# Performance work log

Measured on AMD Instinct MI355X. Metric: run time of the kernel, lower is better.

Reference implementation:

```python
import jax, jax.numpy as jnp
import numpy as np

DIM = 1024
NUM_HEADS = 16
HEAD_DIM = DIM // NUM_HEADS
SCALE = HEAD_DIM ** -0.5


def setup_inputs() -> dict:
    key = jax.random.key(0)
    k1, k2, k3 = jax.random.split(key, 3)
    B, N = 2, 2048
    x = jax.random.normal(k1, (B, N, DIM), dtype=jnp.float32)
    w_qkv = jax.random.normal(k2, (3 * DIM, DIM), dtype=jnp.float32) * (DIM ** -0.5)
    w_proj = jax.random.normal(k3, (DIM, DIM), dtype=jnp.float32) * (DIM ** -0.5)
    b_proj = jnp.zeros((DIM,), dtype=jnp.float32)
    return {"x": x, "w_qkv": w_qkv, "w_proj": w_proj, "b_proj": b_proj}


def reference(x, w_qkv, w_proj, b_proj):
    B, N, C = x.shape
    # qkv projection (no bias): [B,N,3C] -> [3,B,H,N,Dh]
    qkv = jnp.einsum('bnc,dc->bnd', x, w_qkv)
    qkv = qkv.reshape(B, N, 3, NUM_HEADS, HEAD_DIM).transpose(2, 0, 3, 1, 4)
    q, k, v = qkv[0], qkv[1], qkv[2]
    # scaled dot-product attention (full score matrix, as in source)
    attn = jnp.einsum('bhnd,bhmd->bhnm', q * SCALE, k)
    attn = jax.nn.softmax(attn, axis=-1)
    out = jnp.einsum('bhnm,bhmd->bhnd', attn, v)  # [B,H,N,Dh]
    out = out.transpose(0, 2, 1, 3).reshape(B, N, C)
    return out @ w_proj.T + b_proj
```

## Files before the change

kernel.cpp:

```cpp
#include <hip/hip_runtime.h>

#define DIM   1024
#define NH    16
#define HD    64
#define BATCH 2
#define SEQ   2048
#define MTOT  4096
#define SCALE 0.125f
#define LOG2E 1.44269504088896340736f

typedef __attribute__((ext_vector_type(8))) _Float16 half8_t;
typedef __attribute__((ext_vector_type(4))) _Float16 half4_t;
typedef __attribute__((ext_vector_type(2))) __fp16 pk16x2_t;
typedef __attribute__((ext_vector_type(4))) float f32x4;

union H4 { pk16x2_t h2[2]; half4_t h4; ushort4 us; };

__device__ __forceinline__ float4 ld4(const float* p) { return *(const float4*)p; }

__device__ __forceinline__ unsigned short f2h(float f) {
    _Float16 h = (_Float16)f;
    return *(unsigned short*)&h;
}

__device__ __forceinline__ float fast_exp2(float x) {
#if __has_builtin(__builtin_amdgcn_exp2f)
    return __builtin_amdgcn_exp2f(x);
#else
    return exp2f(x);
#endif
}

__device__ __forceinline__ void gl2lds16(const void* g, void* l) {
    __builtin_amdgcn_global_load_lds(
        (const __attribute__((address_space(1))) unsigned int*)g,
        (__attribute__((address_space(3))) unsigned int*)l, 16, 0, 0);
}

__global__ __launch_bounds__(256) void cvt3(const float* __restrict__ x,
                                            const float* __restrict__ wq,
                                            const float* __restrict__ wp,
                                            unsigned short* __restrict__ xh,
                                            unsigned short* __restrict__ wqh,
                                            unsigned short* __restrict__ wph) {
    size_t i = ((size_t)blockIdx.x * 256 + threadIdx.x) * 4;
    if (i < (size_t)MTOT * DIM) {
        float4 t = ld4(x + i);
        ushort4 o = {f2h(t.x), f2h(t.y), f2h(t.z), f2h(t.w)};
        *(ushort4*)(xh + i) = o;
    }
    if (i < (size_t)3 * DIM * DIM) {
        float4 t = ld4(wq + i);
        ushort4 o = {f2h(t.x), f2h(t.y), f2h(t.z), f2h(t.w)};
        *(ushort4*)(wqh + i) = o;
    }
    if (i < (size_t)DIM * DIM) {
        float4 t = ld4(wp + i);
        ushort4 o = {f2h(t.x), f2h(t.y), f2h(t.z), f2h(t.w)};
        *(ushort4*)(wph + i) = o;
    }
}

__device__ __forceinline__ void gemm128_core(const unsigned short* __restrict__ A,
                                             const unsigned short* __restrict__ B,
                                             int m0, int n0, int K,
                                             unsigned short* As, unsigned short* Bs,
                                             f32x4 acc[4][4]) {
    const int tid  = threadIdx.x;
    const int w    = tid >> 6;
    const int lane = tid & 63;
    const int g = lane >> 4, c = lane & 15;
    const int wr = w >> 1, wc = w & 1;

    const int lr = lane >> 3;
    const int js = lane & 7;
    const int j0 = js ^ lr;
    const unsigned short* gA = A + (size_t)(m0 + w * 32 + lr) * K + j0 * 8;
    const unsigned short* gB = B + (size_t)(n0 + w * 32 + lr) * K + j0 * 8;
    unsigned short* lA = As + w * 32 * 64;
    unsigned short* lB = Bs + w * 32 * 64;

    int aoff[4], boff[4];
    #pragma unroll
    for (int t = 0; t < 4; ++t) {
        aoff[t] = (wr * 64 + t * 16 + c) * 64 + ((g ^ (c & 7)) * 8);
        boff[t] = (wc * 64 + t * 16 + c) * 64 + ((g ^ (c & 7)) * 8);
    }

    for (int kb = 0; kb < K; kb += 64) {
        if (kb) __syncthreads();
        #pragma unroll
        for (int i = 0; i < 4; ++i) {
            gl2lds16(gA + kb + (size_t)(8 * i) * K, lA + i * 512);
            gl2lds16(gB + kb + (size_t)(8 * i) * K, lB + i * 512);
        }
        __syncthreads();
        half8_t af0[4], af1[4], bf0[4], bf1[4];
        #pragma unroll
        for (int t = 0; t < 4; ++t) {
            af0[t] = *(const half8_t*)&As[aoff[t]];
            af1[t] = *(const half8_t*)&As[aoff[t] ^ 32];
            bf0[t] = *(const half8_t*)&Bs[boff[t]];
            bf1[t] = *(const half8_t*)&Bs[boff[t] ^ 32];
        }
        #pragma unroll
        for (int rt = 0; rt < 4; ++rt)
            #pragma unroll
            for (int ct = 0; ct < 4; ++ct)
                acc[rt][ct] = __builtin_amdgcn_mfma_f32_16x16x32_f16(
                    af0[rt], bf0[ct], acc[rt][ct], 0, 0, 0);
        #pragma unroll
        for (int rt = 0; rt < 4; ++rt)
            #pragma unroll
            for (int ct = 0; ct < 4; ++ct)
                acc[rt][ct] = __builtin_amdgcn_mfma_f32_16x16x32_f16(
                    af1[rt], bf1[ct], acc[rt][ct], 0, 0, 0);
    }
}

__global__ __launch_bounds__(256) void qkv_mfma(const unsigned short* __restrict__ xh,
                                                const unsigned short* __restrict__ wqh,
                                                unsigned short* __restrict__ q,
                                                unsigned short* __restrict__ k,
                                                unsigned short* __restrict__ vt) {
    __shared__ unsigned short As[128 * 64];
    __shared__ unsigned short Bs[128 * 64];
    const int m0 = blockIdx.x * 128;
    const int n0 = blockIdx.y * 128;
    f32x4 acc[4][4];
    #pragma unroll
    for (int i = 0; i < 4; ++i)
        #pragma unroll
        for (int jj = 0; jj < 4; ++jj) acc[i][jj] = (f32x4){0.f, 0.f, 0.f, 0.f};

    gemm128_core(xh, wqh, m0, n0, DIM, As, Bs, acc);

    const int tid = threadIdx.x, w = tid >> 6, lane = tid & 63;
    const int g = lane >> 4, c = lane & 15;
    const int wr = w >> 1, wc = w & 1;
    const int which = n0 >> 10;
    const int hh    = ((n0 + wc * 64) & 1023) >> 6;
    const int b     = m0 >> 11;
    const int nb    = m0 & 2047;

    if (which == 2) {
        unsigned short* base = vt + (size_t)(b * NH + hh) * HD * SEQ;
        #pragma unroll
        for (int rt = 0; rt < 4; ++rt)
            #pragma unroll
            for (int ct = 0; ct < 4; ++ct) {
                int n4 = nb + wr * 64 + rt * 16 + 4 * g;
                H4 u;
                u.h2[0] = __builtin_amdgcn_cvt_pkrtz(acc[rt][ct][0], acc[rt][ct][1]);
                u.h2[1] = __builtin_amdgcn_cvt_pkrtz(acc[rt][ct][2], acc[rt][ct][3]);
                *(ushort4*)&base[(size_t)(ct * 16 + c) * SEQ + n4] = u.us;
            }
    } else {
        unsigned short* dst  = (which == 0) ? q : k;
        unsigned short* base = dst + (size_t)(b * NH + hh) * SEQ * HD;
        const float sc = (which == 0) ? SCALE * LOG2E : 1.0f;
        #pragma unroll
        for (int rt = 0; rt < 4; ++rt)
            #pragma unroll
            for (int ct = 0; ct < 4; ++ct)
                #pragma unroll
                for (int r = 0; r < 4; ++r) {
                    int row = nb + wr * 64 + rt * 16 + g * 4 + r;
                    base[(size_t)row * HD + ct * 16 + c] = f2h(acc[rt][ct][r] * sc);
                }
    }
}

__global__ __launch_bounds__(256) void proj_mfma(const unsigned short* __restrict__ aoh,
                                                 const unsigned short* __restrict__ wph,
                                                 const float* __restrict__ bias,
                                                 float* __restrict__ out) {
    __shared__ unsigned short As[128 * 64];
    __shared__ unsigned short Bs[128 * 64];
    const int m0 = blockIdx.x * 128;
    const int n0 = blockIdx.y * 128;
    f32x4 acc[4][4];
    #pragma unroll
    for (int i = 0; i < 4; ++i)
        #pragma unroll
        for (int jj = 0; jj < 4; ++jj) acc[i][jj] = (f32x4){0.f, 0.f, 0.f, 0.f};

    gemm128_core(aoh, wph, m0, n0, DIM, As, Bs, acc);

    const int tid = threadIdx.x, w = tid >> 6, lane = tid & 63;
    const int g = lane >> 4, c = lane & 15;
    const int wr = w >> 1, wc = w & 1;
    float br[4];
    #pragma unroll
    for (int ct = 0; ct < 4; ++ct) br[ct] = bias[n0 + wc * 64 + ct * 16 + c];
    #pragma unroll
    for (int rt = 0; rt < 4; ++rt)
        #pragma unroll
        for (int ct = 0; ct < 4; ++ct)
            #pragma unroll
            for (int r = 0; r < 4; ++r) {
                int row = m0 + wr * 64 + rt * 16 + g * 4 + r;
                out[(size_t)row * DIM + n0 + wc * 64 + ct * 16 + c] =
                    acc[rt][ct][r] + br[ct];
            }
}

__global__ __launch_bounds__(256) void attn_mfma(const unsigned short* __restrict__ q,
                                                 const unsigned short* __restrict__ k,
                                                 const unsigned short* __restrict__ vt,
                                                 unsigned short* __restrict__ aoh) {
    __shared__ unsigned short Ks[128 * 64];
    __shared__ unsigned short Vs[64 * 128];

    const int tid  = threadIdx.x;
    const int w    = tid >> 6;
    const int lane = tid & 63;
    const int g    = lane >> 4;
    const int c    = lane & 15;
    const int qt = blockIdx.x, bh = blockIdx.y;
    const int b = bh >> 4, h = bh & 15;
    const int q0 = qt * 128 + w * 32;

    const unsigned short* qbase = q + ((size_t)bh * SEQ + q0) * HD;
    half8_t qf[2][2];
    #pragma unroll
    for (int s = 0; s < 2; ++s) {
        const unsigned short* qr = qbase + (size_t)(s * 16 + c) * HD + g * 8;
        qf[s][0] = *(const half8_t*)qr;
        qf[s][1] = *(const half8_t*)(qr + 32);
    }

    f32x4 o[2][4];
    #pragma unroll
    for (int s = 0; s < 2; ++s)
        #pragma unroll
        for (int dt = 0; dt < 4; ++dt) o[s][dt] = (f32x4){0.f, 0.f, 0.f, 0.f};
    float rs0 = 0.f, rs1 = 0.f;

    const int lr = lane >> 3, js = lane & 7, j0 = js ^ lr;
    const unsigned short* kg = k + (size_t)bh * SEQ * HD + (size_t)(w * 32 + lr) * HD + j0 * 8;
    unsigned short* lK = Ks + w * 32 * 64;
    const int vlr = lane >> 4, vjs = lane & 15;
    const unsigned short* vg[4];
    #pragma unroll
    for (int i = 0; i < 4; ++i)
        vg[i] = vt + (size_t)bh * HD * SEQ + (size_t)(w * 16 + 4 * i + vlr) * SEQ
                   + (vjs ^ (4 * i + vlr)) * 8;
    unsigned short* lV = Vs + w * 16 * 128;

    int koff[8];
    #pragma unroll
    for (int ct = 0; ct < 8; ++ct)
        koff[ct] = (ct * 16 + c) * 64 + ((g ^ (c & 7)) * 8);

    for (int kt = 0; kt < 16; ++kt) {
        if (kt) __syncthreads();
        const size_t kadv = (size_t)kt * 128 * HD;
        #pragma unroll
        for (int i = 0; i < 4; ++i) {
            gl2lds16(kg + kadv + (size_t)(8 * i) * HD, lK + i * 512);
            gl2lds16(vg[i] + kt * 128,                 lV + i * 512);
        }
        __syncthreads();

        half4_t pf0[8], pf1[8];
        #pragma unroll
        for (int ct = 0; ct < 8; ++ct) {
            half8_t kf0 = *(const half8_t*)&Ks[koff[ct]];
            half8_t kf1 = *(const half8_t*)&Ks[koff[ct] ^ 32];
            f32x4 s0 = __builtin_amdgcn_mfma_f32_16x16x32_f16(kf0, qf[0][0],
                           (f32x4){0.f, 0.f, 0.f, 0.f}, 0, 0, 0);
            s0 = __builtin_amdgcn_mfma_f32_16x16x32_f16(kf1, qf[0][1], s0, 0, 0, 0);
            f32x4 s1 = __builtin_amdgcn_mfma_f32_16x16x32_f16(kf0, qf[1][0],
                           (f32x4){0.f, 0.f, 0.f, 0.f}, 0, 0, 0);
            s1 = __builtin_amdgcn_mfma_f32_16x16x32_f16(kf1, qf[1][1], s1, 0, 0, 0);

            float a0 = fast_exp2(s0[0]), a1 = fast_exp2(s0[1]);
            float a2 = fast_exp2(s0[2]), a3 = fast_exp2(s0[3]);
            rs0 += (a0 + a1) + (a2 + a3);
            H4 u0; u0.h2[0] = __builtin_amdgcn_cvt_pkrtz(a0, a1);
                   u0.h2[1] = __builtin_amdgcn_cvt_pkrtz(a2, a3);
            pf0[ct] = u0.h4;
            float b0 = fast_exp2(s1[0]), b1 = fast_exp2(s1[1]);
            float b2 = fast_exp2(s1[2]), b3 = fast_exp2(s1[3]);
            rs1 += (b0 + b1) + (b2 + b3);
            H4 u1; u1.h2[0] = __builtin_amdgcn_cvt_pkrtz(b0, b1);
                   u1.h2[1] = __builtin_amdgcn_cvt_pkrtz(b2, b3);
            pf1[ct] = u1.h4;
        }

        #pragma unroll
        for (int dt = 0; dt < 4; ++dt) {
            #pragma unroll
            for (int kt2 = 0; kt2 < 8; ++kt2) {
                int voff = (dt * 16 + c) * 128 +
                           (((2 * kt2 + (g >> 1)) ^ c) * 8) + 4 * (g & 1);
                half4_t vf = *(const half4_t*)&Vs[voff];
                o[0][dt] = __builtin_amdgcn_mfma_f32_16x16x16f16(vf, pf0[kt2], o[0][dt], 0, 0, 0);
                o[1][dt] = __builtin_amdgcn_mfma_f32_16x16x16f16(vf, pf1[kt2], o[1][dt], 0, 0, 0);
            }
        }
    }

    rs0 += __shfl_xor(rs0, 16); rs0 += __shfl_xor(rs0, 32);
    rs1 += __shfl_xor(rs1, 16); rs1 += __shfl_xor(rs1, 32);
    const float inv[2] = {1.0f / rs0, 1.0f / rs1};

    #pragma unroll
    for (int s = 0; s < 2; ++s) {
        unsigned short* orow = aoh + ((size_t)b * SEQ + q0 + s * 16 + c) * DIM + h * HD;
        #pragma unroll
        for (int dt = 0; dt < 4; ++dt) {
            H4 u;
            u.h2[0] = __builtin_amdgcn_cvt_pkrtz(o[s][dt][0] * inv[s], o[s][dt][1] * inv[s]);
            u.h2[1] = __builtin_amdgcn_cvt_pkrtz(o[s][dt][2] * inv[s], o[s][dt][3] * inv[s]);
            *(ushort4*)&orow[dt * 16 + 4 * g] = u.us;
        }
    }
}

extern "C" void kernel_launch(void* const* d_in, const int* in_sizes, int n_in,
                              void* d_out, int out_size, void* d_ws, size_t ws_size,
                              hipStream_t stream) {
    const float* x      = (const float*)d_in[0];
    const float* w_qkv  = (const float*)d_in[1];
    const float* w_proj = (const float*)d_in[2];
    const float* b_proj = (const float*)d_in[3];
    float* out = (float*)d_out;

    const size_t per = (size_t)BATCH * NH * SEQ * HD;
    const size_t nwq = (size_t)3 * DIM * DIM;
    const size_t nwp = (size_t)DIM * DIM;
    const size_t need = (5 * per + nwq + nwp) * sizeof(unsigned short);
    if (ws_size < need) return;

    unsigned short* q   = (unsigned short*)d_ws;
    unsigned short* k   = q + per;
    unsigned short* vt  = k + per;
    unsigned short* aoh = vt + per;
    unsigned short* xh  = aoh + per;
    unsigned short* wqh = xh + per;
    unsigned short* wph = wqh + nwq;

    cvt3<<<dim3(4096), 256, 0, stream>>>(x, w_qkv, w_proj, xh, wqh, wph);
    qkv_mfma<<<dim3(32, 24), 256, 0, stream>>>(xh, wqh, q, k, vt);
    attn_mfma<<<dim3(16, 32), 256, 0, stream>>>(q, k, vt, aoh);
    proj_mfma<<<dim3(32, 8), 256, 0, stream>>>(aoh, wph, b_proj, out);
}
```

Before: 177.4 us.

## Enlarge attention KV tiles, interleave PV with scores, shrink proj M tile

The attention kernel now stages 256 keys and values per iteration instead of 128, which halves the number of barrier-separated loads. It also issues the P·V MFMAs right after each score chunk instead of buffering all probabilities first, which lowers register pressure. The projection GEMM switches to 64x128 tiles with an inline K loop, doubling the grid to 512 blocks for better CU occupancy. In exchange, attention LDS use doubles to 64 KB per block, which may reduce how many blocks fit on a CU.

Result: no change. 180.1 us (+1.5%).

```diff
diff --git a/kernel.cpp b/kernel.cpp
--- a/kernel.cpp
+++ b/kernel.cpp
@@ -175,32 +175,76 @@
                                                  const unsigned short* __restrict__ wph,
                                                  const float* __restrict__ bias,
                                                  float* __restrict__ out) {
-    __shared__ unsigned short As[128 * 64];
+    __shared__ unsigned short As[64 * 64];
     __shared__ unsigned short Bs[128 * 64];
-    const int m0 = blockIdx.x * 128;
+    const int m0 = blockIdx.x * 64;
     const int n0 = blockIdx.y * 128;
-    f32x4 acc[4][4];
-    #pragma unroll
-    for (int i = 0; i < 4; ++i)
-        #pragma unroll
-        for (int jj = 0; jj < 4; ++jj) acc[i][jj] = (f32x4){0.f, 0.f, 0.f, 0.f};
-
-    gemm128_core(aoh, wph, m0, n0, DIM, As, Bs, acc);
-
     const int tid = threadIdx.x, w = tid >> 6, lane = tid & 63;
     const int g = lane >> 4, c = lane & 15;
-    const int wr = w >> 1, wc = w & 1;
+    const int wm = w & 1, wn = w >> 1;
+
+    f32x4 acc[2][4];
+    #pragma unroll
+    for (int i = 0; i < 2; ++i)
+        #pragma unroll
+        for (int jj = 0; jj < 4; ++jj) acc[i][jj] = (f32x4){0.f, 0.f, 0.f, 0.f};
+
+    const int lr = lane >> 3, js = lane & 7, j0 = js ^ lr;
+    const unsigned short* gA = aoh + (size_t)(m0 + w * 16 + lr) * DIM + j0 * 8;
+    const unsigned short* gB = wph + (size_t)(n0 + w * 32 + lr) * DIM + j0 * 8;
+    unsigned short* lA = As + w * 16 * 64;
+    unsigned short* lB = Bs + w * 32 * 64;
+
+    int aoff[2], boff[4];
+    #pragma unroll
+    for (int t = 0; t < 2; ++t)
+        aoff[t] = (wm * 32 + t * 16 + c) * 64 + ((g ^ (c & 7)) * 8);
+    #pragma unroll
+    for (int t = 0; t < 4; ++t)
+        boff[t] = (wn * 64 + t * 16 + c) * 64 + ((g ^ (c & 7)) * 8);
+
+    for (int kb = 0; kb < DIM; kb += 64) {
+        if (kb) __syncthreads();
+        #pragma unroll
+        for (int i = 0; i < 2; ++i)
+            gl2lds16(gA + kb + (size_t)(8 * i) * DIM, lA + i * 512);
+        #pragma unroll
+        for (int i = 0; i < 4; ++i)
+            gl2lds16(gB + kb + (size_t)(8 * i) * DIM, lB + i * 512);
+        __syncthreads();
+        half8_t af0[2], af1[2], bf0[4], bf1[4];
+        #pragma unroll
+        for (int t = 0; t < 2; ++t) {
+            af0[t] = *(const half8_t*)&As[aoff[t]];
+            af1[t] = *(const half8_t*)&As[aoff[t] ^ 32];
+        }
+        #pragma unroll
+        for (int t = 0; t < 4; ++t) {
+            bf0[t] = *(const half8_t*)&Bs[boff[t]];
+            bf1[t] = *(const half8_t*)&Bs[boff[t] ^ 32];
+        }
+        #pragma unroll
+        for (int rt = 0; rt < 2; ++rt)
+            #pragma unroll
+            for (int ct = 0; ct < 4; ++ct) {
+                acc[rt][ct] = __builtin_amdgcn_mfma_f32_16x16x32_f16(
+                    af0[rt], bf0[ct], acc[rt][ct], 0, 0, 0);
+                acc[rt][ct] = __builtin_amdgcn_mfma_f32_16x16x32_f16(
+                    af1[rt], bf1[ct], acc[rt][ct], 0, 0, 0);
+            }
+    }
+
     float br[4];
     #pragma unroll
-    for (int ct = 0; ct < 4; ++ct) br[ct] = bias[n0 + wc * 64 + ct * 16 + c];
-    #pragma unroll
-    for (int rt = 0; rt < 4; ++rt)
+    for (int ct = 0; ct < 4; ++ct) br[ct] = bias[n0 + wn * 64 + ct * 16 + c];
+    #pragma unroll
+    for (int rt = 0; rt < 2; ++rt)
         #pragma unroll
         for (int ct = 0; ct < 4; ++ct)
             #pragma unroll
             for (int r = 0; r < 4; ++r) {
-                int row = m0 + wr * 64 + rt * 16 + g * 4 + r;
-                out[(size_t)row * DIM + n0 + wc * 64 + ct * 16 + c] =
+                int row = m0 + wm * 32 + rt * 16 + g * 4 + r;
+                out[(size_t)row * DIM + n0 + wn * 64 + ct * 16 + c] =
                     acc[rt][ct][r] + br[ct];
             }
 }
@@ -209,8 +253,8 @@
                                                  const unsigned short* __restrict__ k,
                                                  const unsigned short* __restrict__ vt,
                                                  unsigned short* __restrict__ aoh) {
-    __shared__ unsigned short Ks[128 * 64];
-    __shared__ unsigned short Vs[64 * 128];
+    __shared__ unsigned short Ks[256 * 64];
+    __shared__ unsigned short Vs[64 * 256];
 
     const int tid  = threadIdx.x;
     const int w    = tid >> 6;
@@ -238,34 +282,33 @@
     float rs0 = 0.f, rs1 = 0.f;
 
     const int lr = lane >> 3, js = lane & 7, j0 = js ^ lr;
-    const unsigned short* kg = k + (size_t)bh * SEQ * HD + (size_t)(w * 32 + lr) * HD + j0 * 8;
-    unsigned short* lK = Ks + w * 32 * 64;
-    const int vlr = lane >> 4, vjs = lane & 15;
-    const unsigned short* vg[4];
-    #pragma unroll
-    for (int i = 0; i < 4; ++i)
-        vg[i] = vt + (size_t)bh * HD * SEQ + (size_t)(w * 16 + 4 * i + vlr) * SEQ
-                   + (vjs ^ (4 * i + vlr)) * 8;
-    unsigned short* lV = Vs + w * 16 * 128;
-
-    int koff[8];
-    #pragma unroll
-    for (int ct = 0; ct < 8; ++ct)
+    const unsigned short* kg = k + (size_t)bh * SEQ * HD + (size_t)(w * 64 + lr) * HD + j0 * 8;
+    unsigned short* lK = Ks + w * 64 * 64;
+    const int dr = lane >> 5, kc = lane & 31;
+    const unsigned short* vb_ = vt + (size_t)bh * HD * SEQ;
+    unsigned short* lV = Vs + w * 16 * 256;
+
+    int koff[16];
+    #pragma unroll
+    for (int ct = 0; ct < 16; ++ct)
         koff[ct] = (ct * 16 + c) * 64 + ((g ^ (c & 7)) * 8);
 
-    for (int kt = 0; kt < 16; ++kt) {
+    for (int kt = 0; kt < 8; ++kt) {
         if (kt) __syncthreads();
-        const size_t kadv = (size_t)kt * 128 * HD;
-        #pragma unroll
-        for (int i = 0; i < 4; ++i) {
+        const size_t kadv = (size_t)kt * 256 * HD;
+        #pragma unroll
+        for (int i = 0; i < 8; ++i)
             gl2lds16(kg + kadv + (size_t)(8 * i) * HD, lK + i * 512);
-            gl2lds16(vg[i] + kt * 128,                 lV + i * 512);
+        #pragma unroll
+        for (int i = 0; i < 8; ++i) {
+            int d = w * 16 + 2 * i + dr;
+            gl2lds16(vb_ + (size_t)d * SEQ + kt * 256 + ((kc ^ (2 * i + dr)) * 8),
+                     lV + i * 512);
         }
         __syncthreads();
 
-        half4_t pf0[8], pf1[8];
-        #pragma unroll
-        for (int ct = 0; ct < 8; ++ct) {
+        #pragma unroll
+        for (int ct = 0; ct < 16; ++ct) {
             half8_t kf0 = *(const half8_t*)&Ks[koff[ct]];
             half8_t kf1 = *(const half8_t*)&Ks[koff[ct] ^ 32];
             f32x4 s0 = __builtin_amdgcn_mfma_f32_16x16x32_f16(kf0, qf[0][0],
@@ -280,24 +323,19 @@
             rs0 += (a0 + a1) + (a2 + a3);
             H4 u0; u0.h2[0] = __builtin_amdgcn_cvt_pkrtz(a0, a1);
                    u0.h2[1] = __builtin_amdgcn_cvt_pkrtz(a2, a3);
-            pf0[ct] = u0.h4;
             float b0 = fast_exp2(s1[0]), b1 = fast_exp2(s1[1]);
             float b2 = fast_exp2(s1[2]), b3 = fast_exp2(s1[3]);
             rs1 += (b0 + b1) + (b2 + b3);
             H4 u1; u1.h2[0] = __builtin_amdgcn_cvt_pkrtz(b0, b1);
                    u1.h2[1] = __builtin_amdgcn_cvt_pkrtz(b2, b3);
-            pf1[ct] = u1.h4;
-        }
-
-        #pragma unroll
-        for (int dt = 0; dt < 4; ++dt) {
-            #pragma unroll
-            for (int kt2 = 0; kt2 < 8; ++kt2) {
-                int voff = (dt * 16 + c) * 128 +
-                           (((2 * kt2 + (g >> 1)) ^ c) * 8) + 4 * (g & 1);
+
+            #pragma unroll
+            for (int dt = 0; dt < 4; ++dt) {
+                int voff = (dt * 16 + c) * 256 +
+                           (((2 * ct + (g >> 1)) ^ c) * 8) + 4 * (g & 1);
                 half4_t vf = *(const half4_t*)&Vs[voff];
-                o[0][dt] = __builtin_amdgcn_mfma_f32_16x16x16f16(vf, pf0[kt2], o[0][dt], 0, 0, 0);
-                o[1][dt] = __builtin_amdgcn_mfma_f32_16x16x16f16(vf, pf1[kt2], o[1][dt], 0, 0, 0);
+                o[0][dt] = __builtin_amdgcn_mfma_f32_16x16x16f16(vf, u0.h4, o[0][dt], 0, 0, 0);
+                o[1][dt] = __builtin_amdgcn_mfma_f32_16x16x16f16(vf, u1.h4, o[1][dt], 0, 0, 0);
             }
         }
     }
@@ -345,5 +383,5 @@
     cvt3<<<dim3(4096), 256, 0, stream>>>(x, w_qkv, w_proj, xh, wqh, wph);
     qkv_mfma<<<dim3(32, 24), 256, 0, stream>>>(xh, wqh, q, k, vt);
     attn_mfma<<<dim3(16, 32), 256, 0, stream>>>(q, k, vt, aoh);
-    proj_mfma<<<dim3(32, 8), 256, 0, stream>>>(aoh, wph, b_proj, out);
-}
+    proj_mfma<<<dim3(64, 8), 256, 0, stream>>>(aoh, wph, b_proj, out);
+}
```
